# Performance work log

Measured on AMD Instinct MI355X. Metric: run time of the kernel, lower is better.

Reference implementation:

```python
import jax, jax.numpy as jnp
import numpy as np

N_DOMAINS = 4          # number of unique domain labels in d
NUM_PROJ = 50          # hard-coded in DiscriminativeSlicedWasserstein.__init__
P_POW = 2              # hard-coded p=2


def setup_inputs() -> dict:
    key = jax.random.key(0)
    k1, k2, k3 = jax.random.split(key, 3)
    N, IN_DIM, OUT_DIM = 32768, 2048, 512
    z = jax.random.normal(k1, (N, IN_DIM), dtype=jnp.float32)
    W = jax.random.normal(k2, (IN_DIM, OUT_DIM), dtype=jnp.float32) * 0.02
    b = jnp.zeros((OUT_DIM,), dtype=jnp.float32)
    # random projections on the unit sphere (rows normalized), as in rand_projections
    P = jax.random.normal(k3, (NUM_PROJ, OUT_DIM), dtype=jnp.float32)
    P = P / jnp.sqrt(jnp.sum(P * P, axis=1, keepdims=True))
    # sorted, equal-count domain labels -> grouping becomes a static reshape
    d = jnp.repeat(jnp.arange(N_DOMAINS, dtype=jnp.int32), N // N_DOMAINS)
    return {"z": z, "W": W, "b": b, "P": P, "d": d}


def reference(z, W, b, P, d):
    # z = self.D(z): linear discriminator
    h = z @ W + b                                   # [N, out_dim]
    per = h.shape[0] // N_DOMAINS
    groups = h.reshape(N_DOMAINS, per, -1)          # [G, n, out_dim] (d is sorted equal-count)
    # project each group onto the random directions: z.matmul(P.T)
    proj = jnp.einsum('gnd,kd->gnk', groups, P)     # [G, n, num_proj]
    # sort along the sample axis (torch sorts each projection's values)
    srt = jnp.sort(proj, axis=1)                    # [G, n, num_proj]
    # all domain pairs (itertools.combinations); equal group sizes => mean of
    # per-pair means == mean over the stacked pair differences
    ii, jj = np.triu_indices(N_DOMAINS, k=1)
    diff = srt[jj] - srt[ii]                        # [n_pairs, n, num_proj]
    loss = jnp.mean(diff ** P_POW)
    return loss
```

## Files before the change

kernel.cpp:

```cpp
#include <hip/hip_runtime.h>

#define NROWS 32768
#define KDIM  2048
#define DDIM  512
#define NPROJ 50
#define NDOM  4
#define NPER  8192
#define BNPAD 64
#define PELEM ((size_t)NDOM * NPROJ * NPER)

typedef __attribute__((ext_vector_type(8))) short short8v;
typedef __attribute__((ext_vector_type(4))) float f32x4;

__device__ inline ushort bf16_rne(float x) {
  union { float f; unsigned u; } v; v.f = x;
  unsigned r = v.u + 0x7FFF + ((v.u >> 16) & 1);
  return (ushort)(r >> 16);
}
__device__ inline float bf16_f32(ushort h) {
  union { unsigned u; float f; } v; v.u = ((unsigned)h) << 16;
  return v.f;
}

__global__ __launch_bounds__(256) void wp_kernel(const float* __restrict__ W,
                                                 const float* __restrict__ b,
                                                 const float* __restrict__ P,
                                                 ushort* __restrict__ Bpk,
                                                 float* __restrict__ bp) {
  int idx = blockIdx.x * 256 + threadIdx.x;
  if (idx >= (KDIM + 1) * BNPAD) return;
  int i = idx >> 6;
  int c = idx & 63;
  float acc = 0.f;
  if (c < NPROJ) {
    const float4* row = (const float4*)((i < KDIM) ? (W + (size_t)i * DDIM) : b);
    const float4* pr  = (const float4*)(P + (size_t)c * DDIM);
#pragma unroll 4
    for (int d = 0; d < DDIM / 4; ++d) {
      float4 w = row[d], p = pr[d];
      acc += w.x * p.x + w.y * p.y + w.z * p.z + w.w * p.w;
    }
  }
  if (i < KDIM) {
    int tg = i >> 5, kb = (i >> 3) & 3, e = i & 7;
    int m = c & 15, cf = c >> 4;
    size_t pos = (size_t)(tg * 4 + cf) * 1024 + (kb * 16 + m) * 8 + e;
    ushort h = bf16_rne(acc);
    Bpk[pos]       = h;
    Bpk[pos + 512] = bf16_rne(acc - bf16_f32(h));
  } else {
    bp[c] = acc;
  }
}

__device__ __forceinline__ void split8_trunc(const float4 f0, const float4 f1,
                                             short8v& hi, short8v& lo) {
  const float a[8] = {f0.x, f0.y, f0.z, f0.w, f1.x, f1.y, f1.z, f1.w};
  union { unsigned u[4]; short8v s; } H, L;
#pragma unroll
  for (int p = 0; p < 4; ++p) {
    float a0 = a[2 * p], a1 = a[2 * p + 1];
    unsigned u0 = __float_as_uint(a0), u1 = __float_as_uint(a1);
    H.u[p] = __builtin_amdgcn_perm(u1, u0, 0x07060302);
    float l0 = a0 - __uint_as_float(u0 & 0xFFFF0000u);
    float l1 = a1 - __uint_as_float(u1 & 0xFFFF0000u);
    L.u[p] = __builtin_amdgcn_perm(__float_as_uint(l1), __float_as_uint(l0), 0x07060302);
  }
  hi = H.s; lo = L.s;
}

__device__ __forceinline__ void gload16(const float* g, float* l) {
  __builtin_amdgcn_global_load_lds(
      (const __attribute__((address_space(1))) unsigned int*)(unsigned long long)g,
      (__attribute__((address_space(3))) unsigned int*)(unsigned int)(unsigned long long)l,
      16, 0, 0);
}

__global__ __launch_bounds__(512) void gemm_mfma(const float* __restrict__ z,
                                                 const ushort* __restrict__ Bpk,
                                                 const float* __restrict__ bp,
                                                 float* __restrict__ part) {
  constexpr int KSLICE = KDIM / 4;
  constexpr int NSTEP  = KSLICE / 32;
  __shared__ __align__(16) float A_lds[2][256 * 32];
  __shared__ __align__(16) float B_lds[2][2048];

  const int tid  = threadIdx.x;
  const int lane = tid & 63;
  const int wave = tid >> 6;
  const int m    = lane & 15;
  const int kb   = lane >> 4;
  const int row0 = blockIdx.x * 256;
  const int ksb  = blockIdx.y;
  const int k0   = ksb * KSLICE;

  const float* gsrcA[4];
  const float* Bf = (const float*)Bpk;
#pragma unroll
  for (int a = 0; a < 4; ++a) {
    const int r = wave * 32 + a * 8 + (lane >> 3);
    const int q = (lane & 7) ^ ((lane >> 3) & 7);
    gsrcA[a] = z + (size_t)(row0 + r) * KDIM + k0 + q * 4;
  }
  const float* gsrcB = Bf + (size_t)(k0 >> 5) * 2048 + wave * 256 + lane * 4;

#define STAGE(buf_, t_)                                                      \
  {                                                                          \
    _Pragma("unroll")                                                        \
    for (int a = 0; a < 4; ++a)                                              \
      gload16(gsrcA[a] + (t_) * 32, &A_lds[buf_][(wave * 32 + a * 8) * 32]); \
    gload16(gsrcB + (size_t)(t_) * 2048, &B_lds[buf_][wave * 256]);          \
  }

  f32x4 acc[2][4];
#pragma unroll
  for (int rf = 0; rf < 2; ++rf)
#pragma unroll
    for (int cf = 0; cf < 4; ++cf) acc[rf][cf] = (f32x4)0.f;

  STAGE(0, 0);
  __syncthreads();

#pragma unroll 2
  for (int t = 0; t < NSTEP; ++t) {
    const int buf = t & 1;

    float4 f[2][2];
#pragma unroll
    for (int rf = 0; rf < 2; ++rf) {
      const int r = wave * 32 + rf * 16 + m;
      const float* base = &A_lds[buf][r * 32];
      f[rf][0] = *(const float4*)(base + (((kb * 2)     ^ (m & 7)) * 4));
      f[rf][1] = *(const float4*)(base + (((kb * 2 + 1) ^ (m & 7)) * 4));
    }
    short8v bh[4], bl[4];
    const ushort* Bu = (const ushort*)&B_lds[buf][0];
#pragma unroll
    for (int cf = 0; cf < 4; ++cf) {
      const ushort* fb = Bu + cf * 1024 + lane * 8;
      bh[cf] = *(const short8v*)fb;
      bl[cf] = *(const short8v*)(fb + 512);
    }
    __builtin_amdgcn_sched_barrier(0);

    if (t < NSTEP - 1) STAGE(buf ^ 1, t + 1);
    __builtin_amdgcn_sched_barrier(0);

    short8v ah[2], al[2];
#pragma unroll
    for (int rf = 0; rf < 2; ++rf)
      split8_trunc(f[rf][0], f[rf][1], ah[rf], al[rf]);

#pragma unroll
    for (int cf = 0; cf < 4; ++cf)
#pragma unroll
      for (int rf = 0; rf < 2; ++rf) {
        acc[rf][cf] = __builtin_amdgcn_mfma_f32_16x16x32_bf16(ah[rf], bh[cf], acc[rf][cf], 0, 0, 0);
        acc[rf][cf] = __builtin_amdgcn_mfma_f32_16x16x32_bf16(al[rf], bh[cf], acc[rf][cf], 0, 0, 0);
        acc[rf][cf] = __builtin_amdgcn_mfma_f32_16x16x32_bf16(ah[rf], bl[cf], acc[rf][cf], 0, 0, 0);
      }

    __syncthreads();
  }
#undef STAGE

  const int g = row0 >> 13;
#pragma unroll
  for (int rf = 0; rf < 2; ++rf) {
    const int nbase = (row0 & (NPER - 1)) + wave * 32 + rf * 16 + kb * 4;
#pragma unroll
    for (int cf = 0; cf < 4; ++cf) {
      const int col = cf * 16 + m;
      if (col < NPROJ) {
        const float bj = (ksb == 0) ? bp[col] : 0.f;
        float* dst = part + (size_t)ksb * PELEM +
                     (size_t)(g * NPROJ + col) * NPER + nbase;
        dst[0] = acc[rf][cf][0] + bj;
        dst[1] = acc[rf][cf][1] + bj;
        dst[2] = acc[rf][cf][2] + bj;
        dst[3] = acc[rf][cf][3] + bj;
      }
    }
  }
}

#define CE(a, b, asc) { float x_ = v[a], y_ = v[b]; \
  if ((asc) ? (x_ > y_) : (x_ < y_)) { v[a] = y_; v[b] = x_; } }

__device__ inline int swz(int i) { return i ^ (((i >> 5) & 7) << 2); }
#define SPAD 8192

template <int JMAX>
__device__ inline void wave_merge(float v[8], int t, int k) {
  const bool asc = (((t << 3) & k) == 0);
#pragma unroll
  for (int j = JMAX; j >= 8; j >>= 1) {
    const int d = j >> 3;
    const bool keepmin = (asc != ((t & d) != 0));
#pragma unroll
    for (int e = 0; e < 8; ++e) {
      float o = __shfl_xor(v[e], d, 64);
      v[e] = keepmin ? fminf(v[e], o) : fmaxf(v[e], o);
    }
  }
  CE(0, 4, asc); CE(1, 5, asc); CE(2, 6, asc); CE(3, 7, asc);
  CE(0, 2, asc); CE(1, 3, asc); CE(4, 6, asc); CE(5, 7, asc);
  CE(0, 1, asc); CE(2, 3, asc); CE(4, 5, asc); CE(6, 7, asc);
}

__global__ __launch_bounds__(1024) void sort_cols(float* __restrict__ p0,
                                                  const float* __restrict__ p1,
                                                  const float* __restrict__ p2,
                                                  const float* __restrict__ p3) {
  __shared__ __align__(16) float sA[SPAD];
  __shared__ __align__(16) float sB[SPAD];
  float* col = p0 + (size_t)blockIdx.x * NPER;
  const int t  = threadIdx.x;
  const int i0 = t << 3;
  float v[8];

  *(float4*)&v[0] = *(const float4*)(col + i0);
  *(float4*)&v[4] = *(const float4*)(col + i0 + 4);
  {
    const float* c1 = p1 + (size_t)blockIdx.x * NPER;
    const float* c2 = p2 + (size_t)blockIdx.x * NPER;
    const float* c3 = p3 + (size_t)blockIdx.x * NPER;
    float4 a0 = *(const float4*)(c1 + i0), a1 = *(const float4*)(c1 + i0 + 4);
    float4 b0 = *(const float4*)(c2 + i0), b1 = *(const float4*)(c2 + i0 + 4);
    float4 d0 = *(const float4*)(c3 + i0), d1 = *(const float4*)(c3 + i0 + 4);
    v[0] += a0.x + b0.x + d0.x; v[1] += a0.y + b0.y + d0.y;
    v[2] += a0.z + b0.z + d0.z; v[3] += a0.w + b0.w + d0.w;
    v[4] += a1.x + b1.x + d1.x; v[5] += a1.y + b1.y + d1.y;
    v[6] += a1.z + b1.z + d1.z; v[7] += a1.w + b1.w + d1.w;
  }

  CE(0, 1, true);  CE(2, 3, false); CE(4, 5, true);  CE(6, 7, false);
  CE(0, 2, true);  CE(1, 3, true);  CE(4, 6, false); CE(5, 7, false);
  CE(0, 1, true);  CE(2, 3, true);  CE(4, 5, false); CE(6, 7, false);
  {
    bool d8 = (t & 1) == 0;
    CE(0, 4, d8); CE(1, 5, d8); CE(2, 6, d8); CE(3, 7, d8);
    CE(0, 2, d8); CE(1, 3, d8); CE(4, 6, d8); CE(5, 7, d8);
    CE(0, 1, d8); CE(2, 3, d8); CE(4, 5, d8); CE(6, 7, d8);
  }

  wave_merge<8>(v, t, 16);
  wave_merge<16>(v, t, 32);
  wave_merge<32>(v, t, 64);
  wave_merge<64>(v, t, 128);
  wave_merge<128>(v, t, 256);
  wave_merge<256>(v, t, 512);

  *(float4*)&sA[swz(i0)]     = *(float4*)&v[0];
  *(float4*)&sA[swz(i0 + 4)] = *(float4*)&v[4];
  __syncthreads();
  int cur = 0;

  for (int k = 1024; k <= NPER; k <<= 1) {
    const bool asc = ((i0 & k) == 0);
    for (int j = k >> 1; j >= 512; j >>= 1) {
      const float* src = cur ? sB : sA;
      float*       dst = cur ? sA : sB;
      const int ip = i0 ^ j;
      float4 a0 = *(const float4*)&src[swz(i0)];
      float4 a1 = *(const float4*)&src[swz(i0 + 4)];
      float4 b0 = *(const float4*)&src[swz(ip)];
      float4 b1 = *(const float4*)&src[swz(ip + 4)];
      const bool keepmin = (asc != ((i0 & j) != 0));
      float4 r0, r1;
      if (keepmin) {
        r0.x = fminf(a0.x, b0.x); r0.y = fminf(a0.y, b0.y); r0.z = fminf(a0.z, b0.z); r0.w = fminf(a0.w, b0.w);
        r1.x = fminf(a1.x, b1.x); r1.y = fminf(a1.y, b1.y); r1.z = fminf(a1.z, b1.z); r1.w = fminf(a1.w, b1.w);
      } else {
        r0.x = fmaxf(a0.x, b0.x); r0.y = fmaxf(a0.y, b0.y); r0.z = fmaxf(a0.z, b0.z); r0.w = fmaxf(a0.w, b0.w);
        r1.x = fmaxf(a1.x, b1.x); r1.y = fmaxf(a1.y, b1.y); r1.z = fmaxf(a1.z, b1.z); r1.w = fmaxf(a1.w, b1.w);
      }
      *(float4*)&dst[swz(i0)]     = r0;
      *(float4*)&dst[swz(i0 + 4)] = r1;
      __syncthreads();
      cur ^= 1;
      *(float4*)&v[0] = r0;
      *(float4*)&v[4] = r1;
    }
    wave_merge<256>(v, t, k);
    if (k != NPER) {
      float* d2 = cur ? sB : sA;
      *(float4*)&d2[swz(i0)]     = *(float4*)&v[0];
      *(float4*)&d2[swz(i0 + 4)] = *(float4*)&v[4];
      __syncthreads();
    }
  }

  *(float4*)(col + i0)     = *(float4*)&v[0];
  *(float4*)(col + i0 + 4) = *(float4*)&v[4];
}

__global__ __launch_bounds__(256) void reduce_k(const float* __restrict__ projT,
                                                float* __restrict__ partial) {
  const int k  = blockIdx.x;
  const int nc = blockIdx.y;
  const int n  = nc * 1024 + threadIdx.x * 4;
  const float4 x0 = *(const float4*)(projT + (size_t)(0 * NPROJ + k) * NPER + n);
  const float4 x1 = *(const float4*)(projT + (size_t)(1 * NPROJ + k) * NPER + n);
  const float4 x2 = *(const float4*)(projT + (size_t)(2 * NPROJ + k) * NPER + n);
  const float4 x3 = *(const float4*)(projT + (size_t)(3 * NPROJ + k) * NPER + n);
  const float a0[4] = {x0.x, x0.y, x0.z, x0.w};
  const float a1[4] = {x1.x, x1.y, x1.z, x1.w};
  const float a2[4] = {x2.x, x2.y, x2.z, x2.w};
  const float a3[4] = {x3.x, x3.y, x3.z, x3.w};
  float local = 0.f;
#pragma unroll
  for (int e = 0; e < 4; ++e) {
    float d01 = a0[e] - a1[e], d02 = a0[e] - a2[e], d03 = a0[e] - a3[e];
    float d12 = a1[e] - a2[e], d13 = a1[e] - a3[e], d23 = a2[e] - a3[e];
    local += d01 * d01 + d02 * d02 + d03 * d03 + d12 * d12 + d13 * d13 + d23 * d23;
  }
#pragma unroll
  for (int o = 32; o > 0; o >>= 1) local += __shfl_down(local, o, 64);
  __shared__ float red[4];
  if ((threadIdx.x & 63) == 0) red[threadIdx.x >> 6] = local;
  __syncthreads();
  if (threadIdx.x == 0) partial[nc * NPROJ + k] = red[0] + red[1] + red[2] + red[3];
}

__global__ __launch_bounds__(512) void final_k(const float* __restrict__ partial,
                                               float* __restrict__ out) {
  const int t = threadIdx.x;
  float v = (t < 8 * NPROJ) ? partial[t] : 0.f;
#pragma unroll
  for (int o = 32; o > 0; o >>= 1) v += __shfl_down(v, o, 64);
  __shared__ float red[8];
  if ((t & 63) == 0) red[t >> 6] = v;
  __syncthreads();
  if (t == 0) {
    float s = 0.f;
#pragma unroll
    for (int w = 0; w < 8; ++w) s += red[w];
    out[0] = s * (1.0f / (6.0f * NPER * NPROJ));
  }
}

extern "C" void kernel_launch(void* const* d_in, const int* in_sizes, int n_in,
                              void* d_out, int out_size, void* d_ws, size_t ws_size,
                              hipStream_t stream) {
  const float* z = (const float*)d_in[0];
  const float* W = (const float*)d_in[1];
  const float* b = (const float*)d_in[2];
  const float* P = (const float*)d_in[3];

  float*  part0   = (float*)d_ws;
  float*  part1   = part0 + PELEM;
  float*  part2   = part1 + PELEM;
  float*  part3   = part2 + PELEM;
  ushort* Bpk     = (ushort*)(part3 + PELEM);
  float*  bp      = (float*)(Bpk + (size_t)2 * BNPAD * KDIM);
  float*  partial = bp + BNPAD;

  wp_kernel<<<((KDIM + 1) * BNPAD + 255) / 256, 256, 0, stream>>>(W, b, P, Bpk, bp);
  gemm_mfma<<<dim3(NROWS / 256, 4), 512, 0, stream>>>(z, Bpk, bp, part0);
  sort_cols<<<NDOM * NPROJ, 1024, 0, stream>>>(part0, part1, part2, part3);
  reduce_k<<<dim3(NPROJ, 8), 256, 0, stream>>>(part0, partial);
  final_k<<<1, 512, 0, stream>>>(partial, (float*)d_out);
}
```

Baseline: 140.7 us.

## Shrink GEMM blocks to 128 rows and single-buffer LDS with extra barrier

Halves the GEMM block to 128 rows and 256 threads, doubling the grid, and drops LDS double buffering in favour of one buffer with a barrier between the fragment reads and the next async stage. LDS per block falls from about 80KB to about 20KB, so more blocks can sit on each CU and hide latency through occupancy instead of in-block prefetch. The cost is an extra __syncthreads per k-step, and the next global load now overlaps only the MFMA compute of the current step.

```diff
diff --git a/kernel.cpp b/kernel.cpp
--- a/kernel.cpp
+++ b/kernel.cpp
@@ -76,40 +76,48 @@
       16, 0, 0);
 }
 
-__global__ __launch_bounds__(512) void gemm_mfma(const float* __restrict__ z,
+__global__ __launch_bounds__(256) void gemm_mfma(const float* __restrict__ z,
                                                  const ushort* __restrict__ Bpk,
                                                  const float* __restrict__ bp,
                                                  float* __restrict__ part) {
   constexpr int KSLICE = KDIM / 4;
   constexpr int NSTEP  = KSLICE / 32;
-  __shared__ __align__(16) float A_lds[2][256 * 32];
-  __shared__ __align__(16) float B_lds[2][2048];
+  __shared__ __align__(16) float A_lds[128 * 32];
+  __shared__ __align__(16) float B_lds[2048];
 
   const int tid  = threadIdx.x;
   const int lane = tid & 63;
   const int wave = tid >> 6;
   const int m    = lane & 15;
   const int kb   = lane >> 4;
-  const int row0 = blockIdx.x * 256;
+  const int row0 = blockIdx.x * 128;
   const int ksb  = blockIdx.y;
   const int k0   = ksb * KSLICE;
 
   const float* gsrcA[4];
+  const float* gsrcB[2];
   const float* Bf = (const float*)Bpk;
 #pragma unroll
   for (int a = 0; a < 4; ++a) {
-    const int r = wave * 32 + a * 8 + (lane >> 3);
-    const int q = (lane & 7) ^ ((lane >> 3) & 7);
+    const int j = wave * 4 + a;
+    const int r = j * 8 + (lane >> 3);
+    const int q = (lane & 7) ^ (lane >> 3);
     gsrcA[a] = z + (size_t)(row0 + r) * KDIM + k0 + q * 4;
   }
-  const float* gsrcB = Bf + (size_t)(k0 >> 5) * 2048 + wave * 256 + lane * 4;
-
-#define STAGE(buf_, t_)                                                      \
-  {                                                                          \
-    _Pragma("unroll")                                                        \
-    for (int a = 0; a < 4; ++a)                                              \
-      gload16(gsrcA[a] + (t_) * 32, &A_lds[buf_][(wave * 32 + a * 8) * 32]); \
-    gload16(gsrcB + (size_t)(t_) * 2048, &B_lds[buf_][wave * 256]);          \
+#pragma unroll
+  for (int b2 = 0; b2 < 2; ++b2) {
+    const int j = wave * 2 + b2;
+    gsrcB[b2] = Bf + (size_t)(k0 >> 5) * 2048 + j * 256 + lane * 4;
+  }
+
+#define STAGE(t_)                                                        \
+  {                                                                      \
+    _Pragma("unroll")                                                    \
+    for (int a = 0; a < 4; ++a)                                          \
+      gload16(gsrcA[a] + (t_) * 32, &A_lds[(wave * 4 + a) * 256]);       \
+    _Pragma("unroll")                                                    \
+    for (int b2 = 0; b2 < 2; ++b2)                                       \
+      gload16(gsrcB[b2] + (size_t)(t_) * 2048, &B_lds[(wave * 2 + b2) * 256]); \
   }
 
   f32x4 acc[2][4];
@@ -118,32 +126,29 @@
 #pragma unroll
     for (int cf = 0; cf < 4; ++cf) acc[rf][cf] = (f32x4)0.f;
 
-  STAGE(0, 0);
+  STAGE(0);
   __syncthreads();
 
-#pragma unroll 2
   for (int t = 0; t < NSTEP; ++t) {
-    const int buf = t & 1;
-
     float4 f[2][2];
 #pragma unroll
     for (int rf = 0; rf < 2; ++rf) {
       const int r = wave * 32 + rf * 16 + m;
-      const float* base = &A_lds[buf][r * 32];
+      const float* base = &A_lds[r * 32];
       f[rf][0] = *(const float4*)(base + (((kb * 2)     ^ (m & 7)) * 4));
       f[rf][1] = *(const float4*)(base + (((kb * 2 + 1) ^ (m & 7)) * 4));
     }
     short8v bh[4], bl[4];
-    const ushort* Bu = (const ushort*)&B_lds[buf][0];
+    const ushort* Bu = (const ushort*)&B_lds[0];
 #pragma unroll
     for (int cf = 0; cf < 4; ++cf) {
       const ushort* fb = Bu + cf * 1024 + lane * 8;
       bh[cf] = *(const short8v*)fb;
       bl[cf] = *(const short8v*)(fb + 512);
     }
-    __builtin_amdgcn_sched_barrier(0);
-
-    if (t < NSTEP - 1) STAGE(buf ^ 1, t + 1);
+    __syncthreads();
+
+    if (t < NSTEP - 1) STAGE(t + 1);
     __builtin_amdgcn_sched_barrier(0);
 
     short8v ah[2], al[2];
@@ -357,7 +362,7 @@
   float*  partial = bp + BNPAD;
 
   wp_kernel<<<((KDIM + 1) * BNPAD + 255) / 256, 256, 0, stream>>>(W, b, P, Bpk, bp);
-  gemm_mfma<<<dim3(NROWS / 256, 4), 512, 0, stream>>>(z, Bpk, bp, part0);
+  gemm_mfma<<<dim3(NROWS / 128, 4), 256, 0, stream>>>(z, Bpk, bp, part0);
   sort_cols<<<NDOM * NPROJ, 1024, 0, stream>>>(part0, part1, part2, part3);
   reduce_k<<<dim3(NPROJ, 8), 256, 0, stream>>>(part0, partial);
   final_k<<<1, 512, 0, stream>>>(partial, (float*)d_out);
```

After: 130.5 us. 7.3% less time.
